# Kernel tuning notes

Hardware: AMD Instinct MI355X
Metric: run time of the kernel (lower is better)

The kernel has to match this reference:

```python
import jax, jax.numpy as jnp
import numpy as np

B, S, H, P, T = 8, 2048, 1024, 256, 4
EPS = 1e-12


def setup_inputs() -> dict:
    key = jax.random.key(0)
    ks = jax.random.split(key, 12)
    sd = 0.02
    return {
        "hidden_states": jax.random.normal(ks[0], (B, S, H), jnp.float32),
        "input_tensor": jax.random.normal(ks[1], (B, S, H), jnp.float32),
        "attention_mask": jnp.zeros((B, 1, 1, S), jnp.float32),
        "dense_W": jax.random.normal(ks[2], (H, H), jnp.float32) * sd,
        "dense_b": jnp.zeros((H,), jnp.float32),
        "pal_W1": jax.random.normal(ks[3], (T, H, P), jnp.float32) * sd,  # H2L per task
        "pal_b1": jnp.zeros((T, P), jnp.float32),
        "pal_W2": jax.random.normal(ks[4], (T, P, H), jnp.float32) * sd,  # L2H per task
        "pal_b2": jnp.zeros((T, H), jnp.float32),
        "enc_W": jax.random.normal(ks[5], (H,), jnp.float32) * sd,  # Linear(H,1)
        "enc_b": jnp.zeros((), jnp.float32),
        "sel_W": jax.random.normal(ks[6], (T, H), jnp.float32) * sd,  # Linear(H,T)
        "sel_b": jnp.zeros((T,), jnp.float32),
        "ln_g": jnp.ones((H,), jnp.float32),
        "ln_b": jnp.zeros((H,), jnp.float32),
    }


def reference(hidden_states, input_tensor, attention_mask, dense_W, dense_b,
              pal_W1, pal_b1, pal_W2, pal_b2, enc_W, enc_b, sel_W, sel_b,
              ln_g, ln_b):
    # dense projection (dropout p=0 -> identity)
    h = jnp.einsum('bsh,hk->bsk', hidden_states, dense_W) + dense_b  # [B,S,H]

    # per-task PAL adapters: H -> P -> H, stacked over T
    low = jnp.einsum('bsh,thp->btsp', h, pal_W1) + pal_b1[:, None, :]   # [B,T,S,P]
    task_specific = jnp.einsum('btsp,tph->btsh', low, pal_W2) + pal_b2[:, None, :]  # [B,T,S,H]

    # token-level gating: softmax over sequence of (encoder logits + additive mask)
    task_logits = jnp.einsum('bsh,h->bs', h, enc_W) + enc_b            # [B,S]
    task_weights = jax.nn.softmax(task_logits + attention_mask.reshape(B, S), axis=-1)
    task_vector = jnp.einsum('bs,bsh->bh', task_weights, h)            # [B,H]

    # task selector distribution and weighted combine over task branches
    task_distribution = jax.nn.softmax(task_vector @ sel_W.T + sel_b, axis=-1)  # [B,T]
    summed = jnp.einsum('btsh,bt->bsh', task_specific, task_distribution)       # [B,S,H]

    # residual + LayerNorm (eps=1e-12)
    x = h + input_tensor + summed
    mu = x.mean(-1, keepdims=True)
    var = ((x - mu) ** 2).mean(-1, keepdims=True)
    return ln_g * (x - mu) / jnp.sqrt(var + EPS) + ln_b
```

## Files before the change

### kernel.cpp

```cpp
#include <hip/hip_runtime.h>
#include <stdint.h>

#define DEVI __device__ __forceinline__

typedef __attribute__((ext_vector_type(8))) short s8v;
typedef __attribute__((ext_vector_type(4))) float f4v;
typedef unsigned short u16;

DEVI float bf2f(u16 u) { union { uint32_t i; float f; } c; c.i = ((uint32_t)u) << 16; return c.f; }
DEVI u16 f2bf(float f) {
  union { float f; uint32_t u; } c; c.f = f;
  uint32_t u = c.u;
  u += 0x7fffu + ((u >> 16) & 1u);
  return (u16)(u >> 16);
}

DEVI void gld16(const void* g, void* l) {
  auto gp = reinterpret_cast<const __attribute__((address_space(1))) void*>(reinterpret_cast<uintptr_t>(g));
  auto lp = reinterpret_cast<__attribute__((address_space(3))) void*>(reinterpret_cast<uintptr_t>(l));
  __builtin_amdgcn_global_load_lds(gp, lp, 16, 0, 0);
}

DEVI float wredsum(float v) {
  #pragma unroll
  for (int o = 32; o; o >>= 1) v += __shfl_xor(v, o);
  return v;
}

__global__ void cvt_f32_bf16(const float4* __restrict__ in, ushort4* __restrict__ out) {
  int i = blockIdx.x * 256 + threadIdx.x;
  float4 v = in[i];
  ushort4 o;
  o.x = f2bf(v.x); o.y = f2bf(v.y); o.z = f2bf(v.z); o.w = f2bf(v.w);
  out[i] = o;
}

__global__ void transpose_cvt(const float* __restrict__ in, u16* __restrict__ out, int R, int C) {
  __shared__ float t[32][33];
  in  += (size_t)blockIdx.z * R * C;
  out += (size_t)blockIdx.z * R * C;
  int r0 = blockIdx.y * 32, c0 = blockIdx.x * 32;
  int tx = threadIdx.x, ty = threadIdx.y;
  #pragma unroll
  for (int j = ty; j < 32; j += 8) t[j][tx] = in[(size_t)(r0 + j) * C + c0 + tx];
  __syncthreads();
  #pragma unroll
  for (int j = ty; j < 32; j += 8) out[(size_t)(c0 + j) * R + r0 + tx] = f2bf(t[tx][j]);
}

template<int EPI>
__global__ __launch_bounds__(256, 4) void gemm_bt(
    const u16* __restrict__ A, const u16* __restrict__ Bt, void* out,
    const float* __restrict__ e0, const float* __restrict__ e1, const u16* e2)
{
  const int tid  = threadIdx.x;
  const int lane = tid & 63;
  const int wv   = tid >> 6;
  const int wg = ((blockIdx.x & 7) << 7) | (blockIdx.x >> 3);
  const int tm = wg >> 3;
  const int tn = wg & 7;

  __shared__ char lds[32768];
  char* As = lds;
  char* Bs = lds + 16384;

  f4v acc[4][4];
  #pragma unroll
  for (int i = 0; i < 4; i++)
    #pragma unroll
    for (int j = 0; j < 4; j++) acc[i][j] = f4v{0.f, 0.f, 0.f, 0.f};

  const int wr = wv >> 1, wc = wv & 1;
  const int mB = wr * 64, nB = wc * 64;
  const int fr = lane & 15;
  const int fkbyte = ((lane >> 4) << 3) * 2;

  const char* Ab = (const char*)(A + (size_t)tm * 128 * 1024);
  const char* Bb = (const char*)(Bt + (size_t)tn * 128 * 1024);

  for (int k0 = 0; k0 < 1024; k0 += 64) {
    #pragma unroll
    for (int c = 0; c < 4; ++c) {
      int p = wv * 1024 + lane * 16 + c * 4096;
      int row = p >> 7;
      int kb = (p & 127) ^ ((row & 7) << 4);
      gld16(Ab + (size_t)row * 2048 + k0 * 2 + kb, As + p);
      gld16(Bb + (size_t)row * 2048 + k0 * 2 + kb, Bs + p);
    }
    __syncthreads();
    #pragma unroll
    for (int kk = 0; kk < 2; ++kk) {
      s8v af[4], bf[4];
      #pragma unroll
      for (int i = 0; i < 4; ++i) {
        int ra = mB + i * 16 + fr;
        int rb = nB + i * 16 + fr;
        int kbyte = kk * 64 + fkbyte;
        af[i] = *(const s8v*)(As + ra * 128 + (kbyte ^ ((ra & 7) << 4)));
        bf[i] = *(const s8v*)(Bs + rb * 128 + (kbyte ^ ((rb & 7) << 4)));
      }
      #pragma unroll
      for (int mi = 0; mi < 4; ++mi)
        #pragma unroll
        for (int ni = 0; ni < 4; ++ni)
          acc[mi][ni] = __builtin_amdgcn_mfma_f32_16x16x32_bf16(af[mi], bf[ni], acc[mi][ni], 0, 0, 0);
    }
    __syncthreads();
  }

  const int mBase = tm * 128 + mB;
  const int nBase = tn * 128 + nB;
  const int rl = (lane >> 4) << 2;
  const int cl = lane & 15;
  float scale = 0.f;
  const float* b2row = nullptr;
  if constexpr (EPI == 2) scale = e1[(tm >> 4) * 4 + (tn >> 1)];
  if constexpr (EPI == 3) b2row = e0 + (tm >> 4) * 1024;

  #pragma unroll
  for (int mi = 0; mi < 4; ++mi) {
    #pragma unroll
    for (int ni = 0; ni < 4; ++ni) {
      int n = nBase + ni * 16 + cl;
      #pragma unroll
      for (int v = 0; v < 4; ++v) {
        int m = mBase + mi * 16 + rl + v;
        size_t idx = (size_t)m * 1024 + n;
        float val = acc[mi][ni][v];
        if constexpr (EPI == 1) {
          ((u16*)out)[idx] = f2bf(val + e0[n]);
        } else if constexpr (EPI == 2) {
          ((u16*)out)[idx] = f2bf(scale * (val + e0[n]));
        } else {
          ((u16*)out)[idx] = f2bf(val + b2row[n] + bf2f(e2[idx]) + e1[idx]);
        }
      }
    }
  }
}

__global__ void rowdot_kernel(const u16* __restrict__ h, const float* __restrict__ encW,
                              const float* __restrict__ encb, float* __restrict__ logits) {
  int row  = blockIdx.x * 4 + (threadIdx.x >> 6);
  int lane = threadIdx.x & 63;
  const u16* hp = h + (size_t)row * 1024 + lane * 16;
  s8v a0 = *(const s8v*)hp;
  s8v a1 = *(const s8v*)(hp + 8);
  const float* wp = encW + lane * 16;
  float s = 0.f;
  #pragma unroll
  for (int j = 0; j < 8; j++) s += bf2f((u16)a0[j]) * wp[j];
  #pragma unroll
  for (int j = 0; j < 8; j++) s += bf2f((u16)a1[j]) * wp[8 + j];
  s = wredsum(s);
  if (lane == 0) logits[row] = s + encb[0];
}

__global__ void softmax_seq(const float* __restrict__ logits, const float* __restrict__ mask,
                            float* __restrict__ w) {
  int b = blockIdx.x, tid = threadIdx.x;
  int lane = tid & 63, wv = tid >> 6;
  const float* lp = logits + (size_t)b * 2048;
  const float* mp = mask + (size_t)b * 2048;
  float v[8];
  #pragma unroll
  for (int i = 0; i < 8; i++) v[i] = lp[tid * 8 + i] + mp[tid * 8 + i];
  float mx = -1e30f;
  #pragma unroll
  for (int i = 0; i < 8; i++) mx = fmaxf(mx, v[i]);
  __shared__ float red[4];
  #pragma unroll
  for (int o = 32; o; o >>= 1) mx = fmaxf(mx, __shfl_xor(mx, o));
  if (lane == 0) red[wv] = mx;
  __syncthreads();
  mx = fmaxf(fmaxf(red[0], red[1]), fmaxf(red[2], red[3]));
  __syncthreads();
  float s = 0.f;
  #pragma unroll
  for (int i = 0; i < 8; i++) { v[i] = expf(v[i] - mx); s += v[i]; }
  s = wredsum(s);
  if (lane == 0) red[wv] = s;
  __syncthreads();
  s = red[0] + red[1] + red[2] + red[3];
  float inv = 1.f / s;
  #pragma unroll
  for (int i = 0; i < 8; i++) w[(size_t)b * 2048 + tid * 8 + i] = v[i] * inv;
}

__global__ void taskvec_part(const u16* __restrict__ h, const float* __restrict__ w,
                             float* __restrict__ tvp) {
  int b = blockIdx.y, sc = blockIdx.z;
  int col = blockIdx.x * 256 + threadIdx.x;
  const u16* hp = h + ((size_t)b * 2048 + sc * 256) * 1024 + col;
  const float* wp = w + (size_t)b * 2048 + sc * 256;
  float a0 = 0.f, a1 = 0.f, a2 = 0.f, a3 = 0.f;
  for (int s = 0; s < 256; s += 4) {
    a0 += wp[s]     * bf2f(hp[(size_t)s * 1024]);
    a1 += wp[s + 1] * bf2f(hp[(size_t)(s + 1) * 1024]);
    a2 += wp[s + 2] * bf2f(hp[(size_t)(s + 2) * 1024]);
    a3 += wp[s + 3] * bf2f(hp[(size_t)(s + 3) * 1024]);
  }
  tvp[((size_t)b * 8 + sc) * 1024 + col] = (a0 + a1) + (a2 + a3);
}

__global__ void taskvec_reduce(const float* __restrict__ tvp, float* __restrict__ tv) {
  int b = blockIdx.y;
  int col = blockIdx.x * 256 + threadIdx.x;
  float s = 0.f;
  #pragma unroll
  for (int c = 0; c < 8; c++) s += tvp[((size_t)b * 8 + c) * 1024 + col];
  tv[(size_t)b * 1024 + col] = s;
}

__global__ void taskdist_kernel(const float* __restrict__ tv, const float* __restrict__ selW,
                                const float* __restrict__ selb, const float* __restrict__ pb2,
                                float* __restrict__ dvec, float* __restrict__ bias2) {
  int b = blockIdx.x, tid = threadIdx.x;
  int lane = tid & 63, wv = tid >> 6;
  const float* tp = tv + (size_t)b * 1024;
  const float* sw = selW + (size_t)wv * 1024;
  float s = 0.f;
  #pragma unroll
  for (int j = 0; j < 16; j++) s += tp[lane * 16 + j] * sw[lane * 16 + j];
  s = wredsum(s);
  __shared__ float lg[4];
  if (lane == 0) lg[wv] = s + selb[wv];
  __syncthreads();
  float m = fmaxf(fmaxf(lg[0], lg[1]), fmaxf(lg[2], lg[3]));
  float e0 = expf(lg[0] - m), e1 = expf(lg[1] - m), e2 = expf(lg[2] - m), e3 = expf(lg[3] - m);
  float inv = 1.f / (e0 + e1 + e2 + e3);
  float d0 = e0 * inv, d1 = e1 * inv, d2 = e2 * inv, d3 = e3 * inv;
  if (tid < 4) dvec[b * 4 + tid] = (tid == 0) ? d0 : (tid == 1) ? d1 : (tid == 2) ? d2 : d3;
  #pragma unroll
  for (int c = 0; c < 4; c++) {
    int n = c * 256 + tid;
    bias2[(size_t)b * 1024 + n] =
        d0 * pb2[n] + d1 * pb2[1024 + n] + d2 * pb2[2048 + n] + d3 * pb2[3072 + n];
  }
}

__global__ void ln_bf16_kernel(const u16* __restrict__ x, const float* __restrict__ g,
                               const float* __restrict__ bt, float* __restrict__ out) {
  int row = blockIdx.x, tid = threadIdx.x;
  int lane = tid & 63, wv = tid >> 6;
  ushort4 u = ((const ushort4*)(x + (size_t)row * 1024))[tid];
  float v0 = bf2f(u.x), v1 = bf2f(u.y), v2 = bf2f(u.z), v3 = bf2f(u.w);
  float s = v0 + v1 + v2 + v3;
  float q = v0 * v0 + v1 * v1 + v2 * v2 + v3 * v3;
  #pragma unroll
  for (int o = 32; o; o >>= 1) { s += __shfl_xor(s, o); q += __shfl_xor(q, o); }
  __shared__ float rs[4], rq[4];
  if (lane == 0) { rs[wv] = s; rq[wv] = q; }
  __syncthreads();
  s = rs[0] + rs[1] + rs[2] + rs[3];
  q = rq[0] + rq[1] + rq[2] + rq[3];
  float mu = s * (1.f / 1024.f);
  float var = q * (1.f / 1024.f) - mu * mu;
  float inv = 1.f / sqrtf(var + 1e-12f);
  const float4 gv = ((const float4*)g)[tid];
  const float4 bv = ((const float4*)bt)[tid];
  float4 o;
  o.x = gv.x * (v0 - mu) * inv + bv.x;
  o.y = gv.y * (v1 - mu) * inv + bv.y;
  o.z = gv.z * (v2 - mu) * inv + bv.z;
  o.w = gv.w * (v3 - mu) * inv + bv.w;
  ((float4*)(out + (size_t)row * 1024))[tid] = o;
}

extern "C" void kernel_launch(void* const* d_in, const int* in_sizes, int n_in,
                              void* d_out, int out_size, void* d_ws, size_t ws_size,
                              hipStream_t stream) {
  const float* hidden = (const float*)d_in[0];
  const float* input  = (const float*)d_in[1];
  const float* mask   = (const float*)d_in[2];
  const float* denseW = (const float*)d_in[3];
  const float* denseB = (const float*)d_in[4];
  const float* palW1  = (const float*)d_in[5];
  const float* palB1  = (const float*)d_in[6];
  const float* palW2  = (const float*)d_in[7];
  const float* palB2  = (const float*)d_in[8];
  const float* encW   = (const float*)d_in[9];
  const float* encB   = (const float*)d_in[10];
  const float* selW   = (const float*)d_in[11];
  const float* selB   = (const float*)d_in[12];
  const float* lnG    = (const float*)d_in[13];
  const float* lnB    = (const float*)d_in[14];

  char* ws = (char*)d_ws;
  u16*  hbf    = (u16*)(ws);
  u16*  a0low  = (u16*)(ws + 33554432);
  u16*  wdt    = (u16*)(ws + 67108864);
  u16*  w1t    = (u16*)(ws + 69206016);
  u16*  w2t    = (u16*)(ws + 71303168);
  float* logits = (float*)(ws + 73400320);
  float* wts    = (float*)(ws + 73465856);
  float* tv     = (float*)(ws + 73531392);
  float* dvec   = (float*)(ws + 73564160);
  float* bias2  = (float*)(ws + 73568256);
  float* tvp    = (float*)(ws + 73601024);

  cvt_f32_bf16<<<16384, 256, 0, stream>>>((const float4*)hidden, (ushort4*)a0low);
  transpose_cvt<<<dim3(32, 32, 1), dim3(32, 8), 0, stream>>>(denseW, wdt, 1024, 1024);
  transpose_cvt<<<dim3(8, 32, 4),  dim3(32, 8), 0, stream>>>(palW1, w1t, 1024, 256);
  transpose_cvt<<<dim3(32, 32, 1), dim3(32, 8), 0, stream>>>(palW2, w2t, 1024, 1024);

  gemm_bt<1><<<1024, 256, 0, stream>>>(a0low, wdt, hbf, denseB, nullptr, nullptr);

  rowdot_kernel<<<4096, 256, 0, stream>>>(hbf, encW, encB, logits);
  softmax_seq<<<8, 256, 0, stream>>>(logits, mask, wts);
  taskvec_part<<<dim3(4, 8, 8), 256, 0, stream>>>(hbf, wts, tvp);
  taskvec_reduce<<<dim3(4, 8), 256, 0, stream>>>(tvp, tv);
  taskdist_kernel<<<8, 256, 0, stream>>>(tv, selW, selB, palB2, dvec, bias2);

  gemm_bt<2><<<1024, 256, 0, stream>>>(hbf, w1t, a0low, palB1, dvec, nullptr);
  gemm_bt<3><<<1024, 256, 0, stream>>>(a0low, w2t, hbf, bias2, input, hbf);

  ln_bf16_kernel<<<16384, 256, 0, stream>>>(hbf, lnG, lnB, (float*)d_out);
}
```

Measured before the change: 207.3 us.

## Replace GEMM with 256x256-tile, 8-wave kernel using deep async LDS pipeline

Swaps the 128x128-tile, 4-wave bf16 GEMM for a 256x256-tile, 8-wave kernel. It uses an 8-slot 128KB dynamic-LDS ring filled by global_load_lds seven stages ahead and splits each k-step into four quadrant phases with barriers and setprio around the MFMA bursts. The intent is to raise arithmetic intensity per loaded byte and overlap global loads with MFMA work. In exchange it needs large LDS and many registers (launch bounds 512,2), launches only 256 workgroups (about one per CU), and adds many barriers per iteration.

After: 227.4 us. +9.7%, slower.

```diff
diff --git a/kernel.cpp b/kernel.cpp
--- a/kernel.cpp
+++ b/kernel.cpp
@@ -27,6 +27,8 @@
   return v;
 }
 
+#define MFMA16(a, b, c) __builtin_amdgcn_mfma_f32_16x16x32_bf16((a), (b), (c), 0, 0, 0)
+
 __global__ void cvt_f32_bf16(const float4* __restrict__ in, ushort4* __restrict__ out) {
   int i = blockIdx.x * 256 + threadIdx.x;
   float4 v = in[i];
@@ -49,84 +51,166 @@
 }
 
 template<int EPI>
-__global__ __launch_bounds__(256, 4) void gemm_bt(
+__global__ __launch_bounds__(512, 2) void gemm8p(
     const u16* __restrict__ A, const u16* __restrict__ Bt, void* out,
     const float* __restrict__ e0, const float* __restrict__ e1, const u16* e2)
 {
+  extern __shared__ float4 lds_f4[];
+  char* lds = (char*)lds_f4;
   const int tid  = threadIdx.x;
   const int lane = tid & 63;
-  const int wv   = tid >> 6;
-  const int wg = ((blockIdx.x & 7) << 7) | (blockIdx.x >> 3);
-  const int tm = wg >> 3;
-  const int tn = wg & 7;
-
-  __shared__ char lds[32768];
-  char* As = lds;
-  char* Bs = lds + 16384;
-
-  f4v acc[4][4];
-  #pragma unroll
-  for (int i = 0; i < 4; i++)
-    #pragma unroll
-    for (int j = 0; j < 4; j++) acc[i][j] = f4v{0.f, 0.f, 0.f, 0.f};
-
-  const int wr = wv >> 1, wc = wv & 1;
-  const int mB = wr * 64, nB = wc * 64;
+  const int wid  = tid >> 6;
+  const int wm = wid >> 2, wn = wid & 3;
+
+  const int sw = ((blockIdx.x & 7) << 5) | (blockIdx.x >> 3);
+  const int bn = sw >> 6, bm = sw & 63;
+
   const int fr = lane & 15;
-  const int fkbyte = ((lane >> 4) << 3) * 2;
-
-  const char* Ab = (const char*)(A + (size_t)tm * 128 * 1024);
-  const char* Bb = (const char*)(Bt + (size_t)tn * 128 * 1024);
-
-  for (int k0 = 0; k0 < 1024; k0 += 64) {
-    #pragma unroll
-    for (int c = 0; c < 4; ++c) {
-      int p = wv * 1024 + lane * 16 + c * 4096;
-      int row = p >> 7;
-      int kb = (p & 127) ^ ((row & 7) << 4);
-      gld16(Ab + (size_t)row * 2048 + k0 * 2 + kb, As + p);
-      gld16(Bb + (size_t)row * 2048 + k0 * 2 + kb, Bs + p);
+  const int fk = (lane >> 4) << 4;
+  const int c0 = fk ^ ((fr & 7) << 4);
+
+  const char* Apan = (const char*)A  + (size_t)bm * 256 * 2048;
+  const char* Bpan = (const char*)Bt + (size_t)bn * 256 * 2048;
+
+  const int srow = tid >> 3;
+  const int gcol = ((tid & 7) * 16) ^ ((srow & 7) << 4);
+
+  int aoff[4], boff[2];
+  #pragma unroll
+  for (int i = 0; i < 4; ++i) aoff[i] = (i * 32 + wm * 16 + fr) * 128 + c0;
+  #pragma unroll
+  for (int j = 0; j < 2; ++j) boff[j] = (j * 64 + wn * 16 + fr) * 128 + c0;
+
+  f4v acc[8][4];
+  #pragma unroll
+  for (int i = 0; i < 8; ++i)
+    #pragma unroll
+    for (int j = 0; j < 4; ++j) acc[i][j] = f4v{0.f, 0.f, 0.f, 0.f};
+
+  s8v aR[4][2], bR[4][2];
+
+  auto stage = [&](int h) {
+    const int kt = h >> 2, kind = h & 3;
+    const char* p = (kind == 0 || kind == 3) ? Apan : Bpan;
+    const char* g = p + ((kind >= 2) ? (size_t)(128 * 2048) : 0)
+                      + (size_t)kt * 128 + (size_t)srow * 2048 + gcol;
+    char* l = lds + (size_t)(h & 7) * 16384 + tid * 16;
+    gld16(g, l);
+    gld16(g + (size_t)64 * 2048, l + 8192);
+  };
+
+  #pragma unroll
+  for (int h = 0; h < 7; ++h) stage(h);
+  asm volatile("s_waitcnt vmcnt(6)" ::: "memory");
+  __builtin_amdgcn_s_barrier();
+
+  #pragma unroll 1
+  for (int t = 0; t < 16; ++t) {
+    const int b4 = t * 4;
+    char* sAlo = lds + (size_t)((b4 + 0) & 7) * 16384;
+    char* sBlo = lds + (size_t)((b4 + 1) & 7) * 16384;
+    char* sBhi = lds + (size_t)((b4 + 2) & 7) * 16384;
+    char* sAhi = lds + (size_t)((b4 + 3) & 7) * 16384;
+
+    #pragma unroll
+    for (int i = 0; i < 4; ++i) {
+      aR[i][0] = *(const s8v*)(sAlo + aoff[i]);
+      aR[i][1] = *(const s8v*)(sAlo + (aoff[i] ^ 64));
     }
-    __syncthreads();
-    #pragma unroll
-    for (int kk = 0; kk < 2; ++kk) {
-      s8v af[4], bf[4];
+    #pragma unroll
+    for (int j = 0; j < 2; ++j) {
+      bR[j][0] = *(const s8v*)(sBlo + boff[j]);
+      bR[j][1] = *(const s8v*)(sBlo + (boff[j] ^ 64));
+    }
+    if (t < 15) stage(b4 + 7);
+    __builtin_amdgcn_s_barrier();
+    asm volatile("s_waitcnt lgkmcnt(0)" ::: "memory");
+    __builtin_amdgcn_sched_barrier(0);
+    __builtin_amdgcn_s_setprio(1);
+    #pragma unroll
+    for (int i = 0; i < 4; ++i)
       #pragma unroll
-      for (int i = 0; i < 4; ++i) {
-        int ra = mB + i * 16 + fr;
-        int rb = nB + i * 16 + fr;
-        int kbyte = kk * 64 + fkbyte;
-        af[i] = *(const s8v*)(As + ra * 128 + (kbyte ^ ((ra & 7) << 4)));
-        bf[i] = *(const s8v*)(Bs + rb * 128 + (kbyte ^ ((rb & 7) << 4)));
+      for (int j = 0; j < 2; ++j) {
+        acc[i][j] = MFMA16(aR[i][0], bR[j][0], acc[i][j]);
+        acc[i][j] = MFMA16(aR[i][1], bR[j][1], acc[i][j]);
       }
+    __builtin_amdgcn_s_setprio(0);
+    __builtin_amdgcn_s_barrier();
+
+    #pragma unroll
+    for (int j = 0; j < 2; ++j) {
+      bR[2 + j][0] = *(const s8v*)(sBhi + boff[j]);
+      bR[2 + j][1] = *(const s8v*)(sBhi + (boff[j] ^ 64));
+    }
+    if (t < 14) stage(b4 + 8);
+    __builtin_amdgcn_s_barrier();
+    asm volatile("s_waitcnt lgkmcnt(0)" ::: "memory");
+    __builtin_amdgcn_sched_barrier(0);
+    __builtin_amdgcn_s_setprio(1);
+    #pragma unroll
+    for (int i = 0; i < 4; ++i)
       #pragma unroll
-      for (int mi = 0; mi < 4; ++mi)
-        #pragma unroll
-        for (int ni = 0; ni < 4; ++ni)
-          acc[mi][ni] = __builtin_amdgcn_mfma_f32_16x16x32_bf16(af[mi], bf[ni], acc[mi][ni], 0, 0, 0);
+      for (int j = 2; j < 4; ++j) {
+        acc[i][j] = MFMA16(aR[i][0], bR[j][0], acc[i][j]);
+        acc[i][j] = MFMA16(aR[i][1], bR[j][1], acc[i][j]);
+      }
+    __builtin_amdgcn_s_setprio(0);
+    __builtin_amdgcn_s_barrier();
+
+    #pragma unroll
+    for (int i = 0; i < 4; ++i) {
+      aR[i][0] = *(const s8v*)(sAhi + aoff[i]);
+      aR[i][1] = *(const s8v*)(sAhi + (aoff[i] ^ 64));
     }
-    __syncthreads();
+    if (t < 14) stage(b4 + 9);
+    __builtin_amdgcn_s_barrier();
+    asm volatile("s_waitcnt lgkmcnt(0)" ::: "memory");
+    __builtin_amdgcn_sched_barrier(0);
+    __builtin_amdgcn_s_setprio(1);
+    #pragma unroll
+    for (int i = 0; i < 4; ++i)
+      #pragma unroll
+      for (int j = 0; j < 2; ++j) {
+        acc[4 + i][j] = MFMA16(aR[i][0], bR[j][0], acc[4 + i][j]);
+        acc[4 + i][j] = MFMA16(aR[i][1], bR[j][1], acc[4 + i][j]);
+      }
+    __builtin_amdgcn_s_setprio(0);
+    __builtin_amdgcn_s_barrier();
+
+    if (t < 14) stage(b4 + 10);
+    __builtin_amdgcn_s_barrier();
+    __builtin_amdgcn_sched_barrier(0);
+    __builtin_amdgcn_s_setprio(1);
+    #pragma unroll
+    for (int i = 0; i < 4; ++i)
+      #pragma unroll
+      for (int j = 2; j < 4; ++j) {
+        acc[4 + i][j] = MFMA16(aR[i][0], bR[j][0], acc[4 + i][j]);
+        acc[4 + i][j] = MFMA16(aR[i][1], bR[j][1], acc[4 + i][j]);
+      }
+    __builtin_amdgcn_s_setprio(0);
+    if (t < 14)       { asm volatile("s_waitcnt vmcnt(6)" ::: "memory"); }
+    else if (t == 14) { asm volatile("s_waitcnt vmcnt(0)" ::: "memory"); }
+    __builtin_amdgcn_s_barrier();
   }
 
-  const int mBase = tm * 128 + mB;
-  const int nBase = tn * 128 + nB;
   const int rl = (lane >> 4) << 2;
   const int cl = lane & 15;
   float scale = 0.f;
   const float* b2row = nullptr;
-  if constexpr (EPI == 2) scale = e1[(tm >> 4) * 4 + (tn >> 1)];
-  if constexpr (EPI == 3) b2row = e0 + (tm >> 4) * 1024;
-
-  #pragma unroll
-  for (int mi = 0; mi < 4; ++mi) {
-    #pragma unroll
-    for (int ni = 0; ni < 4; ++ni) {
-      int n = nBase + ni * 16 + cl;
+  if constexpr (EPI == 2) scale = e1[(bm >> 3) * 4 + bn];
+  if constexpr (EPI == 3) b2row = e0 + (size_t)(bm >> 3) * 1024;
+
+  #pragma unroll
+  for (int i = 0; i < 8; ++i) {
+    const int m0 = bm * 256 + (i >> 2) * 128 + (i & 3) * 32 + wm * 16 + rl;
+    #pragma unroll
+    for (int j = 0; j < 4; ++j) {
+      const int n = bn * 256 + (j >> 1) * 128 + (j & 1) * 64 + wn * 16 + cl;
       #pragma unroll
       for (int v = 0; v < 4; ++v) {
-        int m = mBase + mi * 16 + rl + v;
-        size_t idx = (size_t)m * 1024 + n;
-        float val = acc[mi][ni][v];
+        const size_t idx = (size_t)(m0 + v) * 1024 + n;
+        const float val = acc[i][j][v];
         if constexpr (EPI == 1) {
           ((u16*)out)[idx] = f2bf(val + e0[n]);
         } else if constexpr (EPI == 2) {
@@ -299,12 +383,16 @@
   float* bias2  = (float*)(ws + 73568256);
   float* tvp    = (float*)(ws + 73601024);
 
+  (void)hipFuncSetAttribute((const void*)gemm8p<1>, hipFuncAttributeMaxDynamicSharedMemorySize, 131072);
+  (void)hipFuncSetAttribute((const void*)gemm8p<2>, hipFuncAttributeMaxDynamicSharedMemorySize, 131072);
+  (void)hipFuncSetAttribute((const void*)gemm8p<3>, hipFuncAttributeMaxDynamicSharedMemorySize, 131072);
+
   cvt_f32_bf16<<<16384, 256, 0, stream>>>((const float4*)hidden, (ushort4*)a0low);
   transpose_cvt<<<dim3(32, 32, 1), dim3(32, 8), 0, stream>>>(denseW, wdt, 1024, 1024);
   transpose_cvt<<<dim3(8, 32, 4),  dim3(32, 8), 0, stream>>>(palW1, w1t, 1024, 256);
   transpose_cvt<<<dim3(32, 32, 1), dim3(32, 8), 0, stream>>>(palW2, w2t, 1024, 1024);
 
-  gemm_bt<1><<<1024, 256, 0, stream>>>(a0low, wdt, hbf, denseB, nullptr, nullptr);
+  gemm8p<1><<<256, 512, 131072, stream>>>(a0low, wdt, hbf, denseB, nullptr, nullptr);
 
   rowdot_kernel<<<4096, 256, 0, stream>>>(hbf, encW, encB, logits);
   softmax_seq<<<8, 256, 0, stream>>>(logits, mask, wts);
@@ -312,8 +400,8 @@
   taskvec_reduce<<<dim3(4, 8), 256, 0, stream>>>(tvp, tv);
   taskdist_kernel<<<8, 256, 0, stream>>>(tv, selW, selB, palB2, dvec, bias2);
 
-  gemm_bt<2><<<1024, 256, 0, stream>>>(hbf, w1t, a0low, palB1, dvec, nullptr);
-  gemm_bt<3><<<1024, 256, 0, stream>>>(a0low, w2t, hbf, bias2, input, hbf);
+  gemm8p<2><<<256, 512, 131072, stream>>>(hbf, w1t, a0low, palB1, dvec, nullptr);
+  gemm8p<3><<<256, 512, 131072, stream>>>(a0low, w2t, hbf, bias2, input, hbf);
 
   ln_bf16_kernel<<<16384, 256, 0, stream>>>(hbf, lnG, lnB, (float*)d_out);
 }
```

## Double-buffer LDS tiles in PAL adapter GEMMs to overlap loads with MFMA

Applied to the files above, without the earlier changes.

Adds a gemm_db kernel that keeps two LDS buffers per operand and issues the global-to-LDS loads for the next K tile before running the MFMAs on the current one. This halves the number of barriers per K step. It is meant to hide global memory latency behind compute in the two adapter GEMMs. In exchange LDS use doubles to 64KB per block and launch bounds drop to 2 blocks per SM, which lowers occupancy. The dense GEMM still uses the old single-buffered kernel.

Result: slower. 219.1 us (+5.7%).

```diff
diff --git a/kernel.cpp b/kernel.cpp
--- a/kernel.cpp
+++ b/kernel.cpp
@@ -27,6 +27,8 @@
   return v;
 }
 
+#define MFMA16(a, b, c) __builtin_amdgcn_mfma_f32_16x16x32_bf16((a), (b), (c), 0, 0, 0)
+
 __global__ void cvt_f32_bf16(const float4* __restrict__ in, ushort4* __restrict__ out) {
   int i = blockIdx.x * 256 + threadIdx.x;
   float4 v = in[i];
@@ -47,6 +49,7 @@
   #pragma unroll
   for (int j = ty; j < 32; j += 8) out[(size_t)(c0 + j) * R + r0 + tx] = f2bf(t[tx][j]);
 }
+
 
 template<int EPI>
 __global__ __launch_bounds__(256, 4) void gemm_bt(
@@ -73,7 +76,7 @@
   const int wr = wv >> 1, wc = wv & 1;
   const int mB = wr * 64, nB = wc * 64;
   const int fr = lane & 15;
-  const int fkbyte = ((lane >> 4) << 3) * 2;
+  const int fkbyte = (lane >> 4) << 4;
 
   const char* Ab = (const char*)(A + (size_t)tm * 128 * 1024);
   const char* Bb = (const char*)(Bt + (size_t)tn * 128 * 1024);
@@ -103,9 +106,110 @@
       for (int mi = 0; mi < 4; ++mi)
         #pragma unroll
         for (int ni = 0; ni < 4; ++ni)
-          acc[mi][ni] = __builtin_amdgcn_mfma_f32_16x16x32_bf16(af[mi], bf[ni], acc[mi][ni], 0, 0, 0);
+          acc[mi][ni] = MFMA16(af[mi], bf[ni], acc[mi][ni]);
     }
     __syncthreads();
+  }
+
+  const int mBase = tm * 128 + mB;
+  const int nBase = tn * 128 + nB;
+  const int rl = (lane >> 4) << 2;
+  const int cl = lane & 15;
+  float scale = 0.f;
+  const float* b2row = nullptr;
+  if constexpr (EPI == 2) scale = e1[(tm >> 4) * 4 + (tn >> 1)];
+  if constexpr (EPI == 3) b2row = e0 + (tm >> 4) * 1024;
+
+  #pragma unroll
+  for (int mi = 0; mi < 4; ++mi) {
+    #pragma unroll
+    for (int ni = 0; ni < 4; ++ni) {
+      int n = nBase + ni * 16 + cl;
+      #pragma unroll
+      for (int v = 0; v < 4; ++v) {
+        int m = mBase + mi * 16 + rl + v;
+        size_t idx = (size_t)m * 1024 + n;
+        float val = acc[mi][ni][v];
+        if constexpr (EPI == 1) {
+          ((u16*)out)[idx] = f2bf(val + e0[n]);
+        } else if constexpr (EPI == 2) {
+          ((u16*)out)[idx] = f2bf(scale * (val + e0[n]));
+        } else {
+          ((u16*)out)[idx] = f2bf(val + b2row[n] + bf2f(e2[idx]) + e1[idx]);
+        }
+      }
+    }
+  }
+}
+
+template<int EPI>
+__global__ __launch_bounds__(256, 2) void gemm_db(
+    const u16* __restrict__ A, const u16* __restrict__ Bt, void* out,
+    const float* __restrict__ e0, const float* __restrict__ e1, const u16* e2)
+{
+  __shared__ char AsB[2][16384];
+  __shared__ char BsB[2][16384];
+  const int tid  = threadIdx.x;
+  const int lane = tid & 63;
+  const int wv   = tid >> 6;
+  const int wg = ((blockIdx.x & 7) << 7) | (blockIdx.x >> 3);
+  const int tm = wg >> 3;
+  const int tn = wg & 7;
+
+  f4v acc[4][4];
+  #pragma unroll
+  for (int i = 0; i < 4; i++)
+    #pragma unroll
+    for (int j = 0; j < 4; j++) acc[i][j] = f4v{0.f, 0.f, 0.f, 0.f};
+
+  const int wr = wv >> 1, wc = wv & 1;
+  const int mB = wr * 64, nB = wc * 64;
+  const int fr = lane & 15;
+  const int fkbyte = (lane >> 4) << 4;
+
+  const char* Ab = (const char*)(A + (size_t)tm * 128 * 1024);
+  const char* Bb = (const char*)(Bt + (size_t)tn * 128 * 1024);
+
+  auto stage = [&](int buf, int k0) {
+    #pragma unroll
+    for (int c = 0; c < 4; ++c) {
+      int p = wv * 1024 + lane * 16 + c * 4096;
+      int row = p >> 7;
+      int kb = (p & 127) ^ ((row & 7) << 4);
+      gld16(Ab + (size_t)row * 2048 + k0 * 2 + kb, AsB[buf] + p);
+      gld16(Bb + (size_t)row * 2048 + k0 * 2 + kb, BsB[buf] + p);
+    }
+  };
+
+  auto tilestep = [&](int buf, int nextk) {
+    s8v af[4][2], bf[4][2];
+    #pragma unroll
+    for (int kk = 0; kk < 2; ++kk)
+      #pragma unroll
+      for (int i = 0; i < 4; ++i) {
+        int ra = mB + i * 16 + fr;
+        int rb = nB + i * 16 + fr;
+        int kbyte = kk * 64 + fkbyte;
+        af[i][kk] = *(const s8v*)(AsB[buf] + ra * 128 + (kbyte ^ ((ra & 7) << 4)));
+        bf[i][kk] = *(const s8v*)(BsB[buf] + rb * 128 + (kbyte ^ ((rb & 7) << 4)));
+      }
+    if (nextk >= 0) stage(buf ^ 1, nextk);
+    #pragma unroll
+    for (int kk = 0; kk < 2; ++kk)
+      #pragma unroll
+      for (int mi = 0; mi < 4; ++mi)
+        #pragma unroll
+        for (int ni = 0; ni < 4; ++ni)
+          acc[mi][ni] = MFMA16(af[mi][kk], bf[ni][kk], acc[mi][ni]);
+    __syncthreads();
+  };
+
+  stage(0, 0);
+  __syncthreads();
+  #pragma unroll 1
+  for (int t = 0; t < 16; t += 2) {
+    tilestep(0, (t + 1) * 64);
+    tilestep(1, (t + 2 < 16) ? (t + 2) * 64 : -1);
   }
 
   const int mBase = tm * 128 + mB;
@@ -312,8 +416,8 @@
   taskvec_reduce<<<dim3(4, 8), 256, 0, stream>>>(tvp, tv);
   taskdist_kernel<<<8, 256, 0, stream>>>(tv, selW, selB, palB2, dvec, bias2);
 
-  gemm_bt<2><<<1024, 256, 0, stream>>>(hbf, w1t, a0low, palB1, dvec, nullptr);
-  gemm_bt<3><<<1024, 256, 0, stream>>>(a0low, w2t, hbf, bias2, input, hbf);
+  gemm_db<2><<<1024, 256, 0, stream>>>(hbf, w1t, a0low, palB1, dvec, nullptr);
+  gemm_db<3><<<1024, 256, 0, stream>>>(a0low, w2t, hbf, bias2, input, hbf);
 
   ln_bf16_kernel<<<16384, 256, 0, stream>>>(hbf, lnG, lnB, (float*)d_out);
 }
```
